# Kernel tuning notes

Hardware: AMD Instinct MI355X
Metric: run time of the kernel (lower is better)

## Reference

```python
import jax, jax.numpy as jnp
import numpy as np

D_K = 64


def setup_inputs() -> dict:
    key = jax.random.key(0)
    k1, k2, k3 = jax.random.split(key, 3)
    B, H, S, DK, DV = 2, 16, 2048, 64, 64
    Q = jax.random.normal(k1, (B, H, S, DK), dtype=jnp.float32)
    K = jax.random.normal(k2, (B, H, S, DK), dtype=jnp.float32)
    V = jax.random.normal(k3, (B, H, S, DV), dtype=jnp.float32)
    # causal mask, True = keep (broadcasts over batch/head as in the torch code)
    mask = jnp.tril(jnp.ones((S, S), dtype=bool))
    return {"Q": Q, "K": K, "V": V, "mask": mask}


def reference(Q, K, V, mask):
    # scores[b,h,c,v] = sum_k Q[b,h,c,k] * K[b,h,v,k]
    scores = jnp.einsum('bhck,bhvk->bhcv', Q, K)
    # torch: B = inf at ~mask; scores - B  ->  -inf at masked positions
    scores = jnp.where(mask, scores, -jnp.inf)
    # scale applied AFTER masking, exactly as in the torch forward
    probs = jax.nn.softmax(scores / jnp.sqrt(jnp.float32(D_K)), axis=-1)
    return probs @ V
```

## Files before the change

### kernel.cpp

```cpp
#include <hip/hip_runtime.h>

#define S_LEN 2048
#define DIM   64
#define NBH   32
#define QBLK  64
#define KVBLK 64
#define NQT   (S_LEN/QBLK)
#define NPAIR (NQT/2)
#define NBLK  (NBH*NPAIR)

typedef __attribute__((ext_vector_type(4))) float f32x4;
typedef __attribute__((ext_vector_type(8))) short s16x8;
typedef __attribute__((ext_vector_type(4))) short s16x4;

#define MFMA_B16(A,B,C) __builtin_amdgcn_mfma_f32_16x16x32_bf16(A,B,C,0,0,0)

__device__ __forceinline__ short f2bf(float x){
  union{float f;unsigned u;} v; v.f=x;
  unsigned r = v.u + 0x7FFFu + ((v.u>>16)&1u);
  return (short)(r>>16);
}
__device__ __forceinline__ float bf2f(short s){
  union{float f;unsigned u;} v; v.u=((unsigned)(unsigned short)s)<<16;
  return v.f;
}
__device__ __forceinline__ int swz(int row){
  return (((row&7) ^ ((row>>2)&7)) << 3);
}

__global__ __launch_bounds__(256) void fattn_fwd(
    const float* __restrict__ Qg, const float* __restrict__ Kg,
    const float* __restrict__ Vg, float* __restrict__ Og)
{
  __shared__ __attribute__((aligned(16))) short Khi[KVBLK*DIM];
  __shared__ __attribute__((aligned(16))) short Klo[KVBLK*DIM];
  __shared__ __attribute__((aligned(16))) short Vt [DIM*KVBLK];
  __shared__ __attribute__((aligned(16))) short Pl [4*16*KVBLK];

  int bid0 = blockIdx.x;
  int bid  = (bid0 & 7) * (NBLK/8) + (bid0 >> 3);
  int bh   = bid / NPAIR;
  int pr   = bid % NPAIR;

  const int tid = threadIdx.x;
  const int w   = tid >> 6;
  const int l   = tid & 63;
  const int l15 = l & 15;
  const int lg  = l >> 4;

  const float* Qb = Qg + (size_t)bh * S_LEN * DIM;
  const float* Kb = Kg + (size_t)bh * S_LEN * DIM;
  const float* Vb = Vg + (size_t)bh * S_LEN * DIM;
  float*       Ob = Og + (size_t)bh * S_LEN * DIM;

  const float SC = 0.125f * 1.44269504088896f;

  for (int half = 0; half < 2; ++half) {
    const int qt = half ? (NQT - 1 - pr) : pr;
    const int q0 = qt * QBLK;
    const int qg = q0 + w * 16 + l15;

    s16x8 qh[2], ql[2];
#pragma unroll
    for (int s = 0; s < 2; ++s) {
      const int dk0 = (lg << 3) + s * 32;
      const float* qp = Qb + (size_t)qg * DIM + dk0;
      float qv[8];
      *(f32x4*)&qv[0] = *(const f32x4*)qp;
      *(f32x4*)&qv[4] = *(const f32x4*)(qp + 4);
#pragma unroll
      for (int j = 0; j < 8; ++j) {
        short h = f2bf(qv[j]);
        qh[s][j] = h;
        ql[s][j] = f2bf(qv[j] - bf2f(h));
      }
    }

    f32x4 o[4];
#pragma unroll
    for (int d = 0; d < 4; ++d) o[d] = f32x4{0.f,0.f,0.f,0.f};
    float m = -INFINITY, lsum = 0.f;

    const int ntiles = qt + 1;
    for (int t = 0; t < ntiles; ++t) {
      const int kv0 = t * KVBLK;
      __syncthreads();
      {
        const int row = tid >> 4;
        const int c4  = (tid & 15) << 2;
#pragma unroll
        for (int i = 0; i < 4; ++i) {
          const int r = row + (i << 4);
          const f32x4 kv4 = *(const f32x4*)(Kb + (size_t)(kv0 + r) * DIM + c4);
          const f32x4 vv4 = *(const f32x4*)(Vb + (size_t)(kv0 + r) * DIM + c4);
          const int cs = c4 ^ swz(r);
          s16x4 kh, kl;
#pragma unroll
          for (int j = 0; j < 4; ++j) {
            short h = f2bf(kv4[j]);
            kh[j] = h;
            kl[j] = f2bf(kv4[j] - bf2f(h));
          }
          *(s16x4*)&Khi[r * DIM + cs] = kh;
          *(s16x4*)&Klo[r * DIM + cs] = kl;
#pragma unroll
          for (int j = 0; j < 4; ++j) {
            const int dv = c4 + j;
            Vt[dv * KVBLK + (r ^ swz(dv))] = f2bf(vv4[j]);
          }
        }
      }
      __syncthreads();

      f32x4 acc[4];
#pragma unroll
      for (int f = 0; f < 4; ++f) acc[f] = f32x4{0.f,0.f,0.f,0.f};
#pragma unroll
      for (int f = 0; f < 4; ++f) {
        const int kr = f * 16 + l15;
#pragma unroll
        for (int s = 0; s < 2; ++s) {
          const int dk = (((lg << 3) + s * 32) ^ swz(kr));
          s16x8 ah = *(const s16x8*)&Khi[kr * DIM + dk];
          s16x8 al = *(const s16x8*)&Klo[kr * DIM + dk];
          acc[f] = MFMA_B16(ah, qh[s], acc[f]);
          acc[f] = MFMA_B16(ah, ql[s], acc[f]);
          acc[f] = MFMA_B16(al, qh[s], acc[f]);
        }
      }

      const bool diag = (t == qt);
      float z[4][4];
#pragma unroll
      for (int f = 0; f < 4; ++f)
#pragma unroll
        for (int r = 0; r < 4; ++r) {
          float zz = acc[f][r] * SC;
          if (diag) {
            const int kvg = kv0 + f * 16 + (lg << 2) + r;
            if (kvg > qg) zz = -INFINITY;
          }
          z[f][r] = zz;
        }

      float pm = z[0][0];
#pragma unroll
      for (int f = 0; f < 4; ++f)
#pragma unroll
        for (int r = 0; r < 4; ++r) pm = fmaxf(pm, z[f][r]);
      pm = fmaxf(pm, __shfl_xor(pm, 16));
      pm = fmaxf(pm, __shfl_xor(pm, 32));
      const float mn = fmaxf(m, pm);
      const float alpha = exp2f(m - mn);
      float p[4][4];
      float rs = 0.f;
#pragma unroll
      for (int f = 0; f < 4; ++f)
#pragma unroll
        for (int r = 0; r < 4; ++r) {
          const float pv = exp2f(z[f][r] - mn);
          p[f][r] = pv;
          rs += pv;
        }
      rs += __shfl_xor(rs, 16);
      rs += __shfl_xor(rs, 32);
      lsum = lsum * alpha + rs;
      m = mn;
#pragma unroll
      for (int d = 0; d < 4; ++d) o[d] *= alpha;

      short* Pw = &Pl[w * 16 * KVBLK];
#pragma unroll
      for (int f = 0; f < 4; ++f) {
        s16x4 pk;
#pragma unroll
        for (int r = 0; r < 4; ++r) pk[r] = f2bf(p[f][r]);
        const int kvc = (f * 16 + (lg << 2)) ^ swz(l15);
        *(s16x4*)&Pw[l15 * KVBLK + kvc] = pk;
      }

#pragma unroll
      for (int s = 0; s < 2; ++s) {
        const int kv8 = (lg << 3) + s * 32;
        s16x8 pf = *(const s16x8*)&Pw[l15 * KVBLK + (kv8 ^ swz(l15))];
#pragma unroll
        for (int d = 0; d < 4; ++d) {
          const int dv = d * 16 + l15;
          s16x8 vf = *(const s16x8*)&Vt[dv * KVBLK + (kv8 ^ swz(dv))];
          o[d] = MFMA_B16(vf, pf, o[d]);
        }
      }
    }

    const float inv = 1.0f / lsum;
#pragma unroll
    for (int d = 0; d < 4; ++d) {
      f32x4 ov;
#pragma unroll
      for (int r = 0; r < 4; ++r) ov[r] = o[d][r] * inv;
      *(f32x4*)(Ob + (size_t)qg * DIM + d * 16 + (lg << 2)) = ov;
    }
  }
}

extern "C" void kernel_launch(void* const* d_in, const int* in_sizes, int n_in,
                              void* d_out, int out_size, void* d_ws, size_t ws_size,
                              hipStream_t stream) {
  const float* Q = (const float*)d_in[0];
  const float* K = (const float*)d_in[1];
  const float* V = (const float*)d_in[2];
  float* O = (float*)d_out;
  fattn_fwd<<<dim3(NBLK), dim3(256), 0, stream>>>(Q, K, V, O);
}
```

Measured before the change: 183.1 us.

## Precompute bf16 K/V tiles in workspace and stream them with async LDS loads

Adds a prep kernel that converts K into hi/lo bf16 split tiles and V into a transposed, swizzled bf16 tile, written once per tile to the workspace. The main kernel then double-buffers these tiles into LDS with global_load_lds while computing. This removes the per-block redundant fp32 loads and conversions of K/V. It also passes P to the PV MFMA through register shuffles instead of an LDS round trip, and skips the rescale when the running max does not change. In exchange it adds a second launch and extra workspace traffic, keeps the old kernel as a fallback when the workspace is too small, and uses one block per q-tile instead of paired tiles.

```diff
diff --git a/kernel.cpp b/kernel.cpp
--- a/kernel.cpp
+++ b/kernel.cpp
@@ -1,13 +1,12 @@
 #include <hip/hip_runtime.h>
+#include <hip/hip_bf16.h>
 
 #define S_LEN 2048
 #define DIM   64
 #define NBH   32
-#define QBLK  64
-#define KVBLK 64
-#define NQT   (S_LEN/QBLK)
-#define NPAIR (NQT/2)
-#define NBLK  (NBH*NPAIR)
+#define NQT   32
+#define TILE_SH 12288
+#define WS_NEED ((size_t)NBH * NQT * TILE_SH * sizeof(short))
 
 typedef __attribute__((ext_vector_type(4))) float f32x4;
 typedef __attribute__((ext_vector_type(8))) short s16x8;
@@ -24,11 +23,216 @@
   union{float f;unsigned u;} v; v.u=((unsigned)(unsigned short)s)<<16;
   return v.f;
 }
+__device__ __forceinline__ unsigned packbf(float a, float b){
+  __hip_bfloat162 h = __float22bfloat162_rn(make_float2(a, b));
+  union { __hip_bfloat162 h; unsigned u; } cv; cv.h = h; return cv.u;
+}
 __device__ __forceinline__ int swz(int row){
   return (((row&7) ^ ((row>>2)&7)) << 3);
 }
 
-__global__ __launch_bounds__(256) void fattn_fwd(
+__global__ __launch_bounds__(256) void prep_kv(
+    const float* __restrict__ K, const float* __restrict__ V, short* __restrict__ W)
+{
+  const int b  = blockIdx.x;
+  const int bh = b >> 5, t = b & 31;
+  const float* Kt = K + ((size_t)bh * S_LEN + t * 64) * DIM;
+  const float* Vt = V + ((size_t)bh * S_LEN + t * 64) * DIM;
+  short* Wt = W + (size_t)b * TILE_SH;
+  const int tid = threadIdx.x;
+#pragma unroll
+  for (int i = 0; i < 2; ++i) {
+    const int m = i * 256 + tid;
+    const int r = m >> 3, g = m & 7;
+    const int c0 = (g << 3) ^ swz(r);
+    float x[8];
+    *(f32x4*)&x[0] = *(const f32x4*)(Kt + r * DIM + c0);
+    *(f32x4*)&x[4] = *(const f32x4*)(Kt + r * DIM + c0 + 4);
+    s16x8 hi, lo;
+#pragma unroll
+    for (int j = 0; j < 8; ++j) {
+      short h = f2bf(x[j]);
+      hi[j] = h;
+      lo[j] = f2bf(x[j] - bf2f(h));
+    }
+    *(s16x8*)&Wt[m * 8]        = hi;
+    *(s16x8*)&Wt[4096 + m * 8] = lo;
+    const int dv = r;
+    const int k0 = (g << 3) ^ swz(dv);
+    s16x8 vv;
+#pragma unroll
+    for (int j = 0; j < 8; ++j) vv[j] = f2bf(Vt[(size_t)(k0 + j) * DIM + dv]);
+    *(s16x8*)&Wt[8192 + m * 8] = vv;
+  }
+}
+
+__device__ __forceinline__ void stage24(const short* __restrict__ src, short* dst,
+                                        int w, int l) {
+#pragma unroll
+  for (int q = 0; q < 6; ++q) {
+    const int off = (q * 4 + w) << 10;
+    __builtin_amdgcn_global_load_lds(
+        (const __attribute__((address_space(1))) unsigned*)((const char*)src + off + l * 16),
+        (__attribute__((address_space(3))) unsigned*)((char*)dst + off),
+        16, 0, 0);
+  }
+}
+
+__global__ __launch_bounds__(256, 4) void fattn_main(
+    const float* __restrict__ Qg, float* __restrict__ Og, const short* __restrict__ W)
+{
+  __shared__ __attribute__((aligned(16))) short buf[2][TILE_SH];
+
+  const int bid0 = blockIdx.x;
+  const int xcd = bid0 & 7, idx = bid0 >> 3;
+  const int bh = (xcd << 2) + (idx >> 5);
+  const int qt = 31 - (idx & 31);
+
+  const int tid = threadIdx.x;
+  const int w = tid >> 6, l = tid & 63;
+  const int l15 = l & 15, lg = l >> 4;
+
+  const short* Wb = W + (size_t)bh * NQT * TILE_SH;
+  const float* Qb = Qg + (size_t)bh * S_LEN * DIM;
+  float*       Ob = Og + (size_t)bh * S_LEN * DIM;
+
+  const int qg = qt * 64 + w * 16 + l15;
+  const float SC = 0.125f * 1.44269504088896f;
+
+  s16x8 qh[2], ql[2];
+#pragma unroll
+  for (int s = 0; s < 2; ++s) {
+    const float* qp = Qb + (size_t)qg * DIM + (lg << 3) + s * 32;
+    float qv[8];
+    *(f32x4*)&qv[0] = *(const f32x4*)qp;
+    *(f32x4*)&qv[4] = *(const f32x4*)(qp + 4);
+#pragma unroll
+    for (int j = 0; j < 8; ++j) {
+      short h = f2bf(qv[j]);
+      qh[s][j] = h;
+      ql[s][j] = f2bf(qv[j] - bf2f(h));
+    }
+  }
+
+  f32x4 o[4];
+#pragma unroll
+  for (int d = 0; d < 4; ++d) o[d] = f32x4{0.f,0.f,0.f,0.f};
+  float m = -INFINITY, lsum = 0.f;
+
+  const int nt = qt + 1;
+  stage24(Wb, buf[0], w, l);
+  __syncthreads();
+  int cur = 0;
+
+  const int src0 = l15 + ((lg & 1) << 5);
+  const int src1 = src0 + 16;
+  const bool hiH = (lg >= 2);
+
+  for (int t = 0; t < nt; ++t) {
+    if (t + 1 < nt) stage24(Wb + (size_t)(t + 1) * TILE_SH, buf[cur ^ 1], w, l);
+
+    const short* bK  = buf[cur];
+    const short* bKl = bK + 4096;
+    const short* bVt = bK + 8192;
+
+    f32x4 acc[4];
+#pragma unroll
+    for (int f = 0; f < 4; ++f) acc[f] = f32x4{0.f,0.f,0.f,0.f};
+#pragma unroll
+    for (int f = 0; f < 4; ++f) {
+      const int kr = f * 16 + l15;
+#pragma unroll
+      for (int s = 0; s < 2; ++s) {
+        const int dk = (((lg << 3) + (s << 5)) ^ swz(kr));
+        s16x8 ah = *(const s16x8*)&bK [kr * DIM + dk];
+        s16x8 al = *(const s16x8*)&bKl[kr * DIM + dk];
+        acc[f] = MFMA_B16(ah, qh[s], acc[f]);
+        acc[f] = MFMA_B16(ah, ql[s], acc[f]);
+        acc[f] = MFMA_B16(al, qh[s], acc[f]);
+      }
+    }
+
+    const bool diag = (t == qt);
+    const int kv0 = t * 64;
+    float pm = -INFINITY;
+#pragma unroll
+    for (int f = 0; f < 4; ++f)
+#pragma unroll
+      for (int r = 0; r < 4; ++r) {
+        float zz = acc[f][r] * SC;
+        if (diag && (kv0 + f * 16 + (lg << 2) + r) > qg) zz = -INFINITY;
+        acc[f][r] = zz;
+        pm = fmaxf(pm, zz);
+      }
+    pm = fmaxf(pm, __shfl_xor(pm, 16));
+    pm = fmaxf(pm, __shfl_xor(pm, 32));
+
+    if (!__all(pm <= m)) {
+      const float mn = fmaxf(m, pm);
+      const float al = exp2f(m - mn);
+      m = mn; lsum *= al;
+#pragma unroll
+      for (int d = 0; d < 4; ++d) o[d] *= al;
+    }
+    float rs = 0.f;
+#pragma unroll
+    for (int f = 0; f < 4; ++f)
+#pragma unroll
+      for (int r = 0; r < 4; ++r) {
+        const float pv = exp2f(acc[f][r] - m);
+        acc[f][r] = pv;
+        rs += pv;
+      }
+    rs += __shfl_xor(rs, 16);
+    rs += __shfl_xor(rs, 32);
+    lsum += rs;
+
+    unsigned U[4][2];
+#pragma unroll
+    for (int f = 0; f < 4; ++f) {
+      U[f][0] = packbf(acc[f][0], acc[f][1]);
+      U[f][1] = packbf(acc[f][2], acc[f][3]);
+    }
+#pragma unroll
+    for (int s = 0; s < 2; ++s) {
+      unsigned a0 = __shfl(U[2*s][0], src0), a1 = __shfl(U[2*s+1][0], src0);
+      unsigned b0 = __shfl(U[2*s][1], src0), b1 = __shfl(U[2*s+1][1], src0);
+      unsigned c0 = __shfl(U[2*s][0], src1), c1 = __shfl(U[2*s+1][0], src1);
+      unsigned d0 = __shfl(U[2*s][1], src1), d1 = __shfl(U[2*s+1][1], src1);
+      union { unsigned u[4]; s16x8 v; } pb;
+      pb.u[0] = hiH ? a1 : a0;
+      pb.u[1] = hiH ? b1 : b0;
+      pb.u[2] = hiH ? c1 : c0;
+      pb.u[3] = hiH ? d1 : d0;
+      const int kv8 = (lg << 3) + (s << 5);
+#pragma unroll
+      for (int d = 0; d < 4; ++d) {
+        const int dv = d * 16 + l15;
+        s16x8 vf = *(const s16x8*)&bVt[dv * DIM + (kv8 ^ swz(dv))];
+        o[d] = MFMA_B16(vf, pb.v, o[d]);
+      }
+    }
+
+    __syncthreads();
+    cur ^= 1;
+  }
+
+  const float inv = 1.0f / lsum;
+#pragma unroll
+  for (int d = 0; d < 4; ++d) {
+    f32x4 ov;
+#pragma unroll
+    for (int r = 0; r < 4; ++r) ov[r] = o[d][r] * inv;
+    *(f32x4*)(Ob + (size_t)qg * DIM + d * 16 + (lg << 2)) = ov;
+  }
+}
+
+#define QBLK  64
+#define KVBLK 64
+#define NPAIR (NQT/2)
+#define NBLK  (NBH*NPAIR)
+
+__global__ __launch_bounds__(256) void fattn_fb(
     const float* __restrict__ Qg, const float* __restrict__ Kg,
     const float* __restrict__ Vg, float* __restrict__ Og)
 {
@@ -41,53 +245,39 @@
   int bid  = (bid0 & 7) * (NBLK/8) + (bid0 >> 3);
   int bh   = bid / NPAIR;
   int pr   = bid % NPAIR;
-
   const int tid = threadIdx.x;
-  const int w   = tid >> 6;
-  const int l   = tid & 63;
-  const int l15 = l & 15;
-  const int lg  = l >> 4;
-
+  const int w = tid >> 6, l = tid & 63, l15 = l & 15, lg = l >> 4;
   const float* Qb = Qg + (size_t)bh * S_LEN * DIM;
   const float* Kb = Kg + (size_t)bh * S_LEN * DIM;
   const float* Vb = Vg + (size_t)bh * S_LEN * DIM;
   float*       Ob = Og + (size_t)bh * S_LEN * DIM;
-
   const float SC = 0.125f * 1.44269504088896f;
 
   for (int half = 0; half < 2; ++half) {
     const int qt = half ? (NQT - 1 - pr) : pr;
-    const int q0 = qt * QBLK;
-    const int qg = q0 + w * 16 + l15;
-
+    const int qg = qt * QBLK + w * 16 + l15;
     s16x8 qh[2], ql[2];
 #pragma unroll
     for (int s = 0; s < 2; ++s) {
-      const int dk0 = (lg << 3) + s * 32;
-      const float* qp = Qb + (size_t)qg * DIM + dk0;
+      const float* qp = Qb + (size_t)qg * DIM + (lg << 3) + s * 32;
       float qv[8];
       *(f32x4*)&qv[0] = *(const f32x4*)qp;
       *(f32x4*)&qv[4] = *(const f32x4*)(qp + 4);
 #pragma unroll
       for (int j = 0; j < 8; ++j) {
-        short h = f2bf(qv[j]);
-        qh[s][j] = h;
-        ql[s][j] = f2bf(qv[j] - bf2f(h));
-      }
-    }
-
+        short h = f2bf(qv[j]); qh[s][j] = h; ql[s][j] = f2bf(qv[j] - bf2f(h));
+      }
+    }
     f32x4 o[4];
 #pragma unroll
     for (int d = 0; d < 4; ++d) o[d] = f32x4{0.f,0.f,0.f,0.f};
     float m = -INFINITY, lsum = 0.f;
-
     const int ntiles = qt + 1;
     for (int t = 0; t < ntiles; ++t) {
       const int kv0 = t * KVBLK;
       __syncthreads();
       {
-        const int row = tid >> 4;
-        const int c4  = (tid & 15) << 2;
+        const int row = tid >> 4, c4 = (tid & 15) << 2;
 #pragma unroll
         for (int i = 0; i < 4; ++i) {
           const int r = row + (i << 4);
@@ -96,22 +286,14 @@
           const int cs = c4 ^ swz(r);
           s16x4 kh, kl;
 #pragma unroll
-          for (int j = 0; j < 4; ++j) {
-            short h = f2bf(kv4[j]);
-            kh[j] = h;
-            kl[j] = f2bf(kv4[j] - bf2f(h));
-          }
+          for (int j = 0; j < 4; ++j) { short h = f2bf(kv4[j]); kh[j] = h; kl[j] = f2bf(kv4[j] - bf2f(h)); }
           *(s16x4*)&Khi[r * DIM + cs] = kh;
           *(s16x4*)&Klo[r * DIM + cs] = kl;
 #pragma unroll
-          for (int j = 0; j < 4; ++j) {
-            const int dv = c4 + j;
-            Vt[dv * KVBLK + (r ^ swz(dv))] = f2bf(vv4[j]);
-          }
+          for (int j = 0; j < 4; ++j) { const int dv = c4 + j; Vt[dv * KVBLK + (r ^ swz(dv))] = f2bf(vv4[j]); }
         }
       }
       __syncthreads();
-
       f32x4 acc[4];
 #pragma unroll
       for (int f = 0; f < 4; ++f) acc[f] = f32x4{0.f,0.f,0.f,0.f};
@@ -120,7 +302,7 @@
         const int kr = f * 16 + l15;
 #pragma unroll
         for (int s = 0; s < 2; ++s) {
-          const int dk = (((lg << 3) + s * 32) ^ swz(kr));
+          const int dk = (((lg << 3) + (s << 5)) ^ swz(kr));
           s16x8 ah = *(const s16x8*)&Khi[kr * DIM + dk];
           s16x8 al = *(const s16x8*)&Klo[kr * DIM + dk];
           acc[f] = MFMA_B16(ah, qh[s], acc[f]);
@@ -128,7 +310,6 @@
           acc[f] = MFMA_B16(al, qh[s], acc[f]);
         }
       }
-
       const bool diag = (t == qt);
       float z[4][4];
 #pragma unroll
@@ -136,13 +317,9 @@
 #pragma unroll
         for (int r = 0; r < 4; ++r) {
           float zz = acc[f][r] * SC;
-          if (diag) {
-            const int kvg = kv0 + f * 16 + (lg << 2) + r;
-            if (kvg > qg) zz = -INFINITY;
-          }
+          if (diag && (kv0 + f * 16 + (lg << 2) + r) > qg) zz = -INFINITY;
           z[f][r] = zz;
         }
-
       float pm = z[0][0];
 #pragma unroll
       for (int f = 0; f < 4; ++f)
@@ -152,23 +329,17 @@
       pm = fmaxf(pm, __shfl_xor(pm, 32));
       const float mn = fmaxf(m, pm);
       const float alpha = exp2f(m - mn);
-      float p[4][4];
-      float rs = 0.f;
+      float p[4][4]; float rs = 0.f;
 #pragma unroll
       for (int f = 0; f < 4; ++f)
 #pragma unroll
-        for (int r = 0; r < 4; ++r) {
-          const float pv = exp2f(z[f][r] - mn);
-          p[f][r] = pv;
-          rs += pv;
-        }
+        for (int r = 0; r < 4; ++r) { const float pv = exp2f(z[f][r] - mn); p[f][r] = pv; rs += pv; }
       rs += __shfl_xor(rs, 16);
       rs += __shfl_xor(rs, 32);
       lsum = lsum * alpha + rs;
       m = mn;
 #pragma unroll
       for (int d = 0; d < 4; ++d) o[d] *= alpha;
-
       short* Pw = &Pl[w * 16 * KVBLK];
 #pragma unroll
       for (int f = 0; f < 4; ++f) {
@@ -178,7 +349,6 @@
         const int kvc = (f * 16 + (lg << 2)) ^ swz(l15);
         *(s16x4*)&Pw[l15 * KVBLK + kvc] = pk;
       }
-
 #pragma unroll
       for (int s = 0; s < 2; ++s) {
         const int kv8 = (lg << 3) + s * 32;
@@ -191,7 +361,6 @@
         }
       }
     }
-
     const float inv = 1.0f / lsum;
 #pragma unroll
     for (int d = 0; d < 4; ++d) {
@@ -210,5 +379,11 @@
   const float* K = (const float*)d_in[1];
   const float* V = (const float*)d_in[2];
   float* O = (float*)d_out;
-  fattn_fwd<<<dim3(NBLK), dim3(256), 0, stream>>>(Q, K, V, O);
-}
+  if (ws_size >= WS_NEED) {
+    short* W = (short*)d_ws;
+    prep_kv  <<<dim3(NBH * NQT), dim3(256), 0, stream>>>(K, V, W);
+    fattn_main<<<dim3(NBH * NQT), dim3(256), 0, stream>>>(Q, O, W);
+  } else {
+    fattn_fb<<<dim3(NBLK), dim3(256), 0, stream>>>(Q, K, V, O);
+  }
+}
```

Result: slower. 197.1 us (+7.7%).
